# Kernel optimization log

Hardware: AMD Instinct MI355X
Metric: run time of the kernel (lower is better)

The kernel has to match this reference:

```python
import math
import jax, jax.numpy as jnp
import numpy as np

B, S, D, H = 4, 1024, 512, 8
DH = D // H  # 64
SQRT_DIM = math.sqrt(D)


def _relative_shift(pos_score):
    # pos_score: [B, H, S, S]
    b, h, s1, s2 = pos_score.shape
    zeros = jnp.zeros((b, h, s1, 1), dtype=pos_score.dtype)
    padded = jnp.concatenate([zeros, pos_score], axis=-1)      # [B,H,S,S+1]
    padded = padded.reshape(b, h, s2 + 1, s1)                  # [B,H,S+1,S]
    return padded[:, :, 1:].reshape(b, h, s1, s2)


def setup_inputs() -> dict:
    key = jax.random.key(0)
    ks = jax.random.split(key, 14)
    std = 0.02
    inp = {
        "query": jax.random.normal(ks[0], (B, S, D), jnp.float32),
        "key": jax.random.normal(ks[1], (B, S, D), jnp.float32),
        "value": jax.random.normal(ks[2], (B, S, D), jnp.float32),
        "pos_embedding": jax.random.normal(ks[3], (B, S, D), jnp.float32),
        # projection weights stored [in, out] so y = x @ W + b
        "Wq": jax.random.normal(ks[4], (D, D), jnp.float32) * std,
        "bq": jnp.zeros((D,), jnp.float32),
        "Wk": jax.random.normal(ks[5], (D, D), jnp.float32) * std,
        "bk": jnp.zeros((D,), jnp.float32),
        "Wv": jax.random.normal(ks[6], (D, D), jnp.float32) * std,
        "bv": jnp.zeros((D,), jnp.float32),
        "Wp": jax.random.normal(ks[7], (D, D), jnp.float32) * std,  # pos_proj, no bias
        "Wo": jax.random.normal(ks[8], (D, D), jnp.float32) * std,
        "bo": jnp.zeros((D,), jnp.float32),
        "u_bias": jax.random.normal(ks[9], (H, DH), jnp.float32) * std,
        "v_bias": jax.random.normal(ks[10], (H, DH), jnp.float32) * std,
    }
    return inp


def reference(query, key, value, pos_embedding, Wq, bq, Wk, bk, Wv, bv, Wp, Wo, bo, u_bias, v_bias):
    b = query.shape[0]
    q = (query @ Wq + bq).reshape(b, -1, H, DH)          # [B,S,H,DH]
    k = (key @ Wk + bk).reshape(b, -1, H, DH)            # [B,T,H,DH]
    v = (value @ Wv + bv).reshape(b, -1, H, DH)          # [B,T,H,DH]
    p = (pos_embedding @ Wp).reshape(b, -1, H, DH)       # [B,T,H,DH]

    # content score: (q + u) . k  -> [B,H,S,T]
    content_score = jnp.einsum('bshd,bthd->bhst', q + u_bias, k)
    # position score: (q + v) . pos -> [B,H,S,T], then relative shift
    pos_score = jnp.einsum('bshd,bthd->bhst', q + v_bias, p)
    pos_score = _relative_shift(pos_score)

    score = (content_score + pos_score) / SQRT_DIM
    attn = jax.nn.softmax(score, axis=-1)                # dropout p=0 (eval)

    context = jnp.einsum('bhst,bthd->bshd', attn, v).reshape(b, -1, D)
    out = context @ Wo + bo
    return (out, attn)
```

## Files before the change

kernel.cpp:

```cpp
#include <hip/hip_runtime.h>

#define B_  4
#define S_  1024
#define D_  512
#define H_  8
#define DH_ 64
#define SCALE 0.044194173824159216f

typedef short bf16x8 __attribute__((ext_vector_type(8)));
typedef float f32x4  __attribute__((ext_vector_type(4)));

__device__ __forceinline__ unsigned short f2bf(float x) {
    union { float f; unsigned int u; } v; v.f = x;
    unsigned int r = v.u + 0x7fffu + ((v.u >> 16) & 1u);
    return (unsigned short)(r >> 16);
}
__device__ __forceinline__ float bf2f(unsigned short h) {
    union { unsigned int u; float f; } v; v.u = ((unsigned int)h) << 16;
    return v.f;
}

__global__ __launch_bounds__(256) void convert_wt_k(
    const float* __restrict__ W0, const float* __restrict__ W1,
    const float* __restrict__ W2, const float* __restrict__ W3,
    const float* __restrict__ W4,
    unsigned short* __restrict__ T0, unsigned short* __restrict__ T1,
    unsigned short* __restrict__ T2, unsigned short* __restrict__ T3,
    unsigned short* __restrict__ T4)
{
    __shared__ float tile[64][65];
    const float* W;
    unsigned short* T;
    switch (blockIdx.z) {
        case 0: W = W0; T = T0; break;
        case 1: W = W1; T = T1; break;
        case 2: W = W2; T = T2; break;
        case 3: W = W3; T = T3; break;
        default: W = W4; T = T4; break;
    }
    const int r0 = blockIdx.y * 64, c0 = blockIdx.x * 64;
    const int tx = threadIdx.x & 63, ty = threadIdx.x >> 6;
#pragma unroll
    for (int it = 0; it < 16; ++it)
        tile[ty + 4 * it][tx] = W[(size_t)(r0 + ty + 4 * it) * 512 + c0 + tx];
    __syncthreads();
#pragma unroll
    for (int it = 0; it < 16; ++it)
        T[(size_t)(c0 + ty + 4 * it) * 512 + r0 + tx] = f2bf(tile[tx][ty + 4 * it]);
}

__global__ __launch_bounds__(256) void proj_all_k(
    const float* __restrict__ Aq_, const float* __restrict__ Ak_,
    const float* __restrict__ Ap_, const float* __restrict__ Av_,
    const unsigned short* __restrict__ WqT, const unsigned short* __restrict__ WkT,
    const unsigned short* __restrict__ WpT, const unsigned short* __restrict__ WvT,
    const float* __restrict__ bq, const float* __restrict__ bk,
    const float* __restrict__ bv,
    const float* __restrict__ ub, const float* __restrict__ vb,
    unsigned short* __restrict__ qu, unsigned short* __restrict__ qv,
    unsigned short* __restrict__ kbf, unsigned short* __restrict__ pbf,
    unsigned short* __restrict__ v2)
{
    __shared__ unsigned short Ab[64][72];
    __shared__ unsigned short Bb[64][72];
    const int mode = blockIdx.z;
    const float* A;
    const unsigned short* BT;
    switch (mode) {
        case 0: A = Aq_; BT = WqT; break;
        case 1: A = Ak_; BT = WkT; break;
        case 2: A = Ap_; BT = WpT; break;
        default: A = Av_; BT = WvT; break;
    }
    const int tid = threadIdx.x;
    const int i0 = blockIdx.x * 64, j0 = blockIdx.y * 64;
    const int w = tid >> 6, lane = tid & 63, l15 = lane & 15, lhi = lane >> 4;
    const int mr0 = (w >> 1) * 32, nc0 = (w & 1) * 32;
    f32x4 acc[2][2] = {};

    for (int k0 = 0; k0 < 512; k0 += 64) {
        __syncthreads();
#pragma unroll
        for (int it = 0; it < 4; ++it) {
            const int s = tid + it * 256;
            const int row = s >> 4, f4 = (s & 15) * 4;
            float4 va = *(const float4*)&A[(size_t)(i0 + row) * 512 + k0 + f4];
            ushort4 hh;
            hh.x = f2bf(va.x); hh.y = f2bf(va.y); hh.z = f2bf(va.z); hh.w = f2bf(va.w);
            *(ushort4*)&Ab[row][f4] = hh;
        }
#pragma unroll
        for (int it = 0; it < 2; ++it) {
            const int s = tid + it * 256;
            const int row = s >> 3, g = (s & 7) * 8;
            *(bf16x8*)&Bb[row][g] = *(const bf16x8*)&BT[(size_t)(j0 + row) * 512 + k0 + g];
        }
        __syncthreads();
#pragma unroll
        for (int kk = 0; kk < 2; ++kk) {
            bf16x8 a0 = *(const bf16x8*)&Ab[mr0 + l15][kk * 32 + lhi * 8];
            bf16x8 a1 = *(const bf16x8*)&Ab[mr0 + 16 + l15][kk * 32 + lhi * 8];
            bf16x8 b0 = *(const bf16x8*)&Bb[nc0 + l15][kk * 32 + lhi * 8];
            bf16x8 b1 = *(const bf16x8*)&Bb[nc0 + 16 + l15][kk * 32 + lhi * 8];
            acc[0][0] = __builtin_amdgcn_mfma_f32_16x16x32_bf16(a0, b0, acc[0][0], 0, 0, 0);
            acc[0][1] = __builtin_amdgcn_mfma_f32_16x16x32_bf16(a0, b1, acc[0][1], 0, 0, 0);
            acc[1][0] = __builtin_amdgcn_mfma_f32_16x16x32_bf16(a1, b0, acc[1][0], 0, 0, 0);
            acc[1][1] = __builtin_amdgcn_mfma_f32_16x16x32_bf16(a1, b1, acc[1][1], 0, 0, 0);
        }
    }

#pragma unroll
    for (int m = 0; m < 2; ++m)
#pragma unroll
        for (int n = 0; n < 2; ++n)
#pragma unroll
            for (int r = 0; r < 4; ++r) {
                const int grow = i0 + mr0 + 16 * m + 4 * lhi + r;
                const int gcol = j0 + nc0 + 16 * n + l15;
                const int b = grow >> 10, s = grow & 1023;
                const int h = gcol >> 6, d = gcol & 63;
                const float v = acc[m][n][r];
                if (mode == 3) {
                    const size_t idx = (((size_t)(b * H_ + h) * 32 + (s >> 5)) * 64 + d) * 32 + (s & 31);
                    v2[idx] = f2bf(v + bv[gcol]);
                } else {
                    const size_t idx = (((size_t)b * H_ + h) * S_ + s) * DH_ + d;
                    if (mode == 0) {
                        const float base = v + bq[gcol];
                        qu[idx] = f2bf(base + ub[gcol]);
                        qv[idx] = f2bf(base + vb[gcol]);
                    } else if (mode == 1) {
                        kbf[idx] = f2bf(v + bk[gcol]);
                    } else {
                        pbf[idx] = f2bf(v);
                    }
                }
            }
}

__global__ __launch_bounds__(256) void gemm_bf16_k(
    const unsigned short* __restrict__ A,
    const unsigned short* __restrict__ BT,
    const float* __restrict__ bias,
    float* __restrict__ C)
{
    __shared__ unsigned short Ab[64][72];
    __shared__ unsigned short Bb[64][72];
    const int tid = threadIdx.x;
    const int i0 = blockIdx.x * 64, j0 = blockIdx.y * 64;
    const int w = tid >> 6, lane = tid & 63, l15 = lane & 15, lhi = lane >> 4;
    const int mr0 = (w >> 1) * 32, nc0 = (w & 1) * 32;
    f32x4 acc[2][2] = {};

    for (int k0 = 0; k0 < 512; k0 += 64) {
        __syncthreads();
#pragma unroll
        for (int it = 0; it < 2; ++it) {
            const int s = tid + it * 256;
            const int row = s >> 3, g = (s & 7) * 8;
            *(bf16x8*)&Ab[row][g] = *(const bf16x8*)&A[(size_t)(i0 + row) * 512 + k0 + g];
            *(bf16x8*)&Bb[row][g] = *(const bf16x8*)&BT[(size_t)(j0 + row) * 512 + k0 + g];
        }
        __syncthreads();
#pragma unroll
        for (int kk = 0; kk < 2; ++kk) {
            bf16x8 a0 = *(const bf16x8*)&Ab[mr0 + l15][kk * 32 + lhi * 8];
            bf16x8 a1 = *(const bf16x8*)&Ab[mr0 + 16 + l15][kk * 32 + lhi * 8];
            bf16x8 b0 = *(const bf16x8*)&Bb[nc0 + l15][kk * 32 + lhi * 8];
            bf16x8 b1 = *(const bf16x8*)&Bb[nc0 + 16 + l15][kk * 32 + lhi * 8];
            acc[0][0] = __builtin_amdgcn_mfma_f32_16x16x32_bf16(a0, b0, acc[0][0], 0, 0, 0);
            acc[0][1] = __builtin_amdgcn_mfma_f32_16x16x32_bf16(a0, b1, acc[0][1], 0, 0, 0);
            acc[1][0] = __builtin_amdgcn_mfma_f32_16x16x32_bf16(a1, b0, acc[1][0], 0, 0, 0);
            acc[1][1] = __builtin_amdgcn_mfma_f32_16x16x32_bf16(a1, b1, acc[1][1], 0, 0, 0);
        }
    }

#pragma unroll
    for (int m = 0; m < 2; ++m)
#pragma unroll
        for (int n = 0; n < 2; ++n)
#pragma unroll
            for (int r = 0; r < 4; ++r) {
                const int grow = i0 + mr0 + 16 * m + 4 * lhi + r;
                const int gcol = j0 + nc0 + 16 * n + l15;
                C[(size_t)grow * 512 + gcol] = acc[m][n][r] + bias[gcol];
            }
}

#define RS 1032
#define QBLK 16

__global__ __launch_bounds__(512, 4) void score_fused_k(
    const unsigned short* __restrict__ qu_g,
    const unsigned short* __restrict__ qv_g,
    const unsigned short* __restrict__ kb_g,
    const unsigned short* __restrict__ pb_g,
    const unsigned short* __restrict__ v2_g,
    float* __restrict__ attn,
    unsigned short* __restrict__ ctx_g)
{
    __shared__ unsigned short Kb[128][72];
    __shared__ unsigned short Pb[128][72];
    __shared__ unsigned short Rsh[16 * RS];
    __shared__ float red[16][9];

    const int tid = threadIdx.x;
    const int i0 = blockIdx.x * QBLK;
    const int bh = blockIdx.y;
    const int w = tid >> 6, lane = tid & 63, l15 = lane & 15, lhi = lane >> 4;

    const unsigned short* qu_b = qu_g + (size_t)bh * S_ * DH_;
    const unsigned short* qv_b = qv_g + (size_t)bh * S_ * DH_;
    const unsigned short* kb_b = kb_g + (size_t)bh * S_ * DH_;
    const unsigned short* pb_b = pb_g + (size_t)bh * S_ * DH_;

    if (tid < 16) {
        const int j = i0 + tid + 1;
        if (j <= 1023) Rsh[tid * RS + j] = 0;
    }

    bf16x8 qf[2], aq0[2], aq1[2];
    {
        const int qrow  = i0 + l15;
        const int qrow1 = min(i0 + 16 + l15, S_ - 1);
#pragma unroll
        for (int kk = 0; kk < 2; ++kk) {
            const int off = kk * 32 + lhi * 8;
            qf[kk]  = *(const bf16x8*)&qu_b[(size_t)qrow  * DH_ + off];
            aq0[kk] = *(const bf16x8*)&qv_b[(size_t)qrow  * DH_ + off];
            aq1[kk] = *(const bf16x8*)&qv_b[(size_t)qrow1 * DH_ + off];
        }
    }

    bf16x8 kreg[2], preg[2];
#pragma unroll
    for (int it = 0; it < 2; ++it) {
        const int s = tid + it * 512;
        const int row = s >> 3, seg = (s & 7) * 8;
        kreg[it] = *(const bf16x8*)&kb_b[(size_t)row * DH_ + seg];
        preg[it] = *(const bf16x8*)&pb_b[(size_t)row * DH_ + seg];
    }

    f32x4 acc[8] = {};
    for (int jc = 0; jc < 8; ++jc) {
        __syncthreads();
#pragma unroll
        for (int it = 0; it < 2; ++it) {
            const int s = tid + it * 512;
            const int row = s >> 3, seg = (s & 7) * 8;
            *(bf16x8*)&Kb[row][seg] = kreg[it];
            *(bf16x8*)&Pb[row][seg] = preg[it];
        }
        if (jc < 7) {
#pragma unroll
            for (int it = 0; it < 2; ++it) {
                const int s = tid + it * 512;
                const int row = (jc + 1) * 128 + (s >> 3), seg = (s & 7) * 8;
                kreg[it] = *(const bf16x8*)&kb_b[(size_t)row * DH_ + seg];
                preg[it] = *(const bf16x8*)&pb_b[(size_t)row * DH_ + seg];
            }
        }
        __syncthreads();

        f32x4 racc0 = {}, racc1 = {};
#pragma unroll
        for (int kk = 0; kk < 2; ++kk) {
            bf16x8 pfr = *(const bf16x8*)&Pb[16 * w + l15][kk * 32 + lhi * 8];
            bf16x8 kfr = *(const bf16x8*)&Kb[16 * w + l15][kk * 32 + lhi * 8];
            racc0 = __builtin_amdgcn_mfma_f32_16x16x32_bf16(aq0[kk], pfr, racc0, 0, 0, 0);
            racc1 = __builtin_amdgcn_mfma_f32_16x16x32_bf16(aq1[kk], pfr, racc1, 0, 0, 0);
            acc[jc] = __builtin_amdgcn_mfma_f32_16x16x32_bf16(qf[kk], kfr, acc[jc], 0, 0, 0);
        }

        const int u = jc * 128 + 16 * w + l15;
#pragma unroll
        for (int r = 0; r < 4; ++r) {
            const int rl = 4 * lhi + r;
            const int gr = i0 + rl;
            const int jlo = u + gr - 1023;
            const unsigned short val = f2bf(racc0[r]);
            if (jlo >= 0)      Rsh[rl * RS + jlo] = val;
            else if (rl >= 1)  Rsh[(rl - 1) * RS + (u + gr + 1)] = val;
        }
        if (lhi == 0) {
            const int jhi = u + i0 + 17;
            if (jhi <= 1023) Rsh[15 * RS + jhi] = f2bf(racc1[0]);
        }
    }
    __syncthreads();

    const int il = 4 * lhi;
    float rmax[4], rsum[4];
#pragma unroll
    for (int r = 0; r < 4; ++r) rmax[r] = -3.0e38f;

#pragma unroll
    for (int jc = 0; jc < 8; ++jc)
#pragma unroll
        for (int r = 0; r < 4; ++r) {
            const int row = il + r;
            const int j = jc * 128 + 16 * w + l15;
            const float pos = bf2f(Rsh[row * RS + j]);
            const float s = (acc[jc][r] + pos) * SCALE;
            acc[jc][r] = s;
            rmax[r] = fmaxf(rmax[r], s);
        }

#pragma unroll
    for (int r = 0; r < 4; ++r)
#pragma unroll
        for (int off = 1; off < 16; off <<= 1)
            rmax[r] = fmaxf(rmax[r], __shfl_xor(rmax[r], off));
    if (l15 == 0)
#pragma unroll
        for (int r = 0; r < 4; ++r) red[il + r][w] = rmax[r];
    __syncthreads();
#pragma unroll
    for (int r = 0; r < 4; ++r) {
        float mx = red[il + r][0];
#pragma unroll
        for (int ww = 1; ww < 8; ++ww) mx = fmaxf(mx, red[il + r][ww]);
        rmax[r] = mx;
        rsum[r] = 0.f;
    }
    __syncthreads();

#pragma unroll
    for (int jc = 0; jc < 8; ++jc)
#pragma unroll
        for (int r = 0; r < 4; ++r) {
            const float e = __expf(acc[jc][r] - rmax[r]);
            acc[jc][r] = e;
            rsum[r] += e;
        }
#pragma unroll
    for (int r = 0; r < 4; ++r)
#pragma unroll
        for (int off = 1; off < 16; off <<= 1)
            rsum[r] += __shfl_xor(rsum[r], off);
    if (l15 == 0)
#pragma unroll
        for (int r = 0; r < 4; ++r) red[il + r][w] = rsum[r];
    __syncthreads();

    float* attn_b = attn + (size_t)bh * S_ * S_;
#pragma unroll
    for (int r = 0; r < 4; ++r) {
        float sum = red[il + r][0];
#pragma unroll
        for (int ww = 1; ww < 8; ++ww) sum += red[il + r][ww];
        const float inv = 1.f / sum;
#pragma unroll
        for (int jc = 0; jc < 8; ++jc) {
            const int j = jc * 128 + 16 * w + l15;
            const float pn = acc[jc][r] * inv;
            attn_b[(size_t)(i0 + il + r) * S_ + j] = pn;
            Rsh[(il + r) * RS + j] = f2bf(pn);
        }
    }
    __syncthreads();

    const int b4 = bh >> 3, h4 = bh & 7;
    const int nblk = w & 3;
    const int kh = w >> 2;
    const unsigned short* v2b = v2_g + (size_t)bh * 32 * 2048;
    const int dd = 16 * nblk + l15;
    f32x4 cacc = {};
#pragma unroll
    for (int half = 0; half < 2; ++half) {
        bf16x8 bbuf[8];
#pragma unroll
        for (int ki = 0; ki < 8; ++ki) {
            const int tb = kh * 16 + half * 8 + ki;
            bbuf[ki] = *(const bf16x8*)&v2b[(size_t)tb * 2048 + dd * 32 + lhi * 8];
        }
#pragma unroll
        for (int ki = 0; ki < 8; ++ki) {
            const int t0 = (kh * 16 + half * 8 + ki) * 32 + lhi * 8;
            bf16x8 a = *(const bf16x8*)&Rsh[l15 * RS + t0];
            cacc = __builtin_amdgcn_mfma_f32_16x16x32_bf16(a, bbuf[ki], cacc, 0, 0, 0);
        }
    }
    float* fred = (float*)&Kb[0][0];
    if (kh == 0) {
#pragma unroll
        for (int r = 0; r < 4; ++r)
            fred[(nblk * 16 + 4 * lhi + r) * 16 + l15] = cacc[r];
    }
    __syncthreads();
    if (kh == 1) {
#pragma unroll
        for (int r = 0; r < 4; ++r) {
            const float vs = cacc[r] + fred[(nblk * 16 + 4 * lhi + r) * 16 + l15];
            const int srow = i0 + 4 * lhi + r;
            ctx_g[((size_t)(b4 * S_ + srow)) * D_ + h4 * DH_ + 16 * nblk + l15] = f2bf(vs);
        }
    }
}

extern "C" void kernel_launch(void* const* d_in, const int* in_sizes, int n_in,
                              void* d_out, int out_size, void* d_ws, size_t ws_size,
                              hipStream_t stream)
{
    const float* query = (const float*)d_in[0];
    const float* key_  = (const float*)d_in[1];
    const float* value = (const float*)d_in[2];
    const float* pose  = (const float*)d_in[3];
    const float* Wq = (const float*)d_in[4];
    const float* bq = (const float*)d_in[5];
    const float* Wk = (const float*)d_in[6];
    const float* bk = (const float*)d_in[7];
    const float* Wv = (const float*)d_in[8];
    const float* bv = (const float*)d_in[9];
    const float* Wp = (const float*)d_in[10];
    const float* Wo = (const float*)d_in[11];
    const float* bo = (const float*)d_in[12];
    const float* u_bias = (const float*)d_in[13];
    const float* v_bias = (const float*)d_in[14];

    const size_t NTOK = (size_t)B_ * S_ * D_;
    float* out  = (float*)d_out;
    float* attn = (float*)d_out + NTOK;

    unsigned short* qu  = (unsigned short*)d_ws;
    unsigned short* qv  = qu + NTOK;
    unsigned short* kbf = qv + NTOK;
    unsigned short* pbf = kbf + NTOK;
    unsigned short* WqT = pbf + NTOK;
    unsigned short* WkT = WqT + 262144;
    unsigned short* WpT = WkT + 262144;
    unsigned short* WvT = WpT + 262144;
    unsigned short* WoT = WvT + 262144;
    unsigned short* v2  = WoT + 262144;
    unsigned short* ctx = v2 + NTOK;

    const dim3 blk256(256);
    const dim3 gproj(64, 8);

    convert_wt_k<<<dim3(8, 8, 5), blk256, 0, stream>>>(Wq, Wk, Wp, Wv, Wo,
                                                       WqT, WkT, WpT, WvT, WoT);

    proj_all_k<<<dim3(64, 8, 4), blk256, 0, stream>>>(
        query, key_, pose, value,
        WqT, WkT, WpT, WvT,
        bq, bk, bv, u_bias, v_bias,
        qu, qv, kbf, pbf, v2);

    score_fused_k<<<dim3(S_ / QBLK, B_ * H_), dim3(512), 0, stream>>>(
        qu, qv, kbf, pbf, v2, attn, ctx);

    gemm_bf16_k<<<gproj, blk256, 0, stream>>>(ctx, WoT, bo, out);
}
```

Measured before the change: 131.8 us.

## Enlarge projection tiles and load K/P fragments directly into registers

The projection GEMM now uses 128x128 tiles with 512 threads, each wave computing 2x4 MFMA tiles, so each loaded fragment is reused more often and fewer blocks are launched. The score kernel no longer stages K and P through shared memory with barriers per chunk. Each wave reads its own MFMA fragments from global memory straight into registers and prefetches the next chunk one step ahead. This cuts LDS traffic and barriers and shrinks shared memory, at the cost of less coalesced global reads and more registers.

```diff
diff --git a/kernel.cpp b/kernel.cpp
--- a/kernel.cpp
+++ b/kernel.cpp
@@ -49,7 +49,7 @@
         T[(size_t)(c0 + ty + 4 * it) * 512 + r0 + tx] = f2bf(tile[tx][ty + 4 * it]);
 }
 
-__global__ __launch_bounds__(256) void proj_all_k(
+__global__ __launch_bounds__(512) void proj_all_k(
     const float* __restrict__ Aq_, const float* __restrict__ Ak_,
     const float* __restrict__ Ap_, const float* __restrict__ Av_,
     const unsigned short* __restrict__ WqT, const unsigned short* __restrict__ WkT,
@@ -61,8 +61,8 @@
     unsigned short* __restrict__ kbf, unsigned short* __restrict__ pbf,
     unsigned short* __restrict__ v2)
 {
-    __shared__ unsigned short Ab[64][72];
-    __shared__ unsigned short Bb[64][72];
+    __shared__ unsigned short Ab[128][72];
+    __shared__ unsigned short Bb[128][72];
     const int mode = blockIdx.z;
     const float* A;
     const unsigned short* BT;
@@ -73,16 +73,16 @@
         default: A = Av_; BT = WvT; break;
     }
     const int tid = threadIdx.x;
-    const int i0 = blockIdx.x * 64, j0 = blockIdx.y * 64;
+    const int i0 = blockIdx.x * 128, j0 = blockIdx.y * 128;
     const int w = tid >> 6, lane = tid & 63, l15 = lane & 15, lhi = lane >> 4;
-    const int mr0 = (w >> 1) * 32, nc0 = (w & 1) * 32;
-    f32x4 acc[2][2] = {};
+    const int mr0 = (w >> 1) * 32, nc0 = (w & 1) * 64;
+    f32x4 acc[2][4] = {};
 
     for (int k0 = 0; k0 < 512; k0 += 64) {
         __syncthreads();
 #pragma unroll
         for (int it = 0; it < 4; ++it) {
-            const int s = tid + it * 256;
+            const int s = tid + it * 512;
             const int row = s >> 4, f4 = (s & 15) * 4;
             float4 va = *(const float4*)&A[(size_t)(i0 + row) * 512 + k0 + f4];
             ushort4 hh;
@@ -91,7 +91,7 @@
         }
 #pragma unroll
         for (int it = 0; it < 2; ++it) {
-            const int s = tid + it * 256;
+            const int s = tid + it * 512;
             const int row = s >> 3, g = (s & 7) * 8;
             *(bf16x8*)&Bb[row][g] = *(const bf16x8*)&BT[(size_t)(j0 + row) * 512 + k0 + g];
         }
@@ -100,19 +100,19 @@
         for (int kk = 0; kk < 2; ++kk) {
             bf16x8 a0 = *(const bf16x8*)&Ab[mr0 + l15][kk * 32 + lhi * 8];
             bf16x8 a1 = *(const bf16x8*)&Ab[mr0 + 16 + l15][kk * 32 + lhi * 8];
-            bf16x8 b0 = *(const bf16x8*)&Bb[nc0 + l15][kk * 32 + lhi * 8];
-            bf16x8 b1 = *(const bf16x8*)&Bb[nc0 + 16 + l15][kk * 32 + lhi * 8];
-            acc[0][0] = __builtin_amdgcn_mfma_f32_16x16x32_bf16(a0, b0, acc[0][0], 0, 0, 0);
-            acc[0][1] = __builtin_amdgcn_mfma_f32_16x16x32_bf16(a0, b1, acc[0][1], 0, 0, 0);
-            acc[1][0] = __builtin_amdgcn_mfma_f32_16x16x32_bf16(a1, b0, acc[1][0], 0, 0, 0);
-            acc[1][1] = __builtin_amdgcn_mfma_f32_16x16x32_bf16(a1, b1, acc[1][1], 0, 0, 0);
+#pragma unroll
+            for (int n = 0; n < 4; ++n) {
+                bf16x8 bn = *(const bf16x8*)&Bb[nc0 + 16 * n + l15][kk * 32 + lhi * 8];
+                acc[0][n] = __builtin_amdgcn_mfma_f32_16x16x32_bf16(a0, bn, acc[0][n], 0, 0, 0);
+                acc[1][n] = __builtin_amdgcn_mfma_f32_16x16x32_bf16(a1, bn, acc[1][n], 0, 0, 0);
+            }
         }
     }
 
 #pragma unroll
     for (int m = 0; m < 2; ++m)
 #pragma unroll
-        for (int n = 0; n < 2; ++n)
+        for (int n = 0; n < 4; ++n)
 #pragma unroll
             for (int r = 0; r < 4; ++r) {
                 const int grow = i0 + mr0 + 16 * m + 4 * lhi + r;
@@ -199,10 +199,9 @@
     float* __restrict__ attn,
     unsigned short* __restrict__ ctx_g)
 {
-    __shared__ unsigned short Kb[128][72];
-    __shared__ unsigned short Pb[128][72];
     __shared__ unsigned short Rsh[16 * RS];
     __shared__ float red[16][9];
+    __shared__ float fred[1024];
 
     const int tid = threadIdx.x;
     const int i0 = blockIdx.x * QBLK;
@@ -232,45 +231,34 @@
         }
     }
 
-    bf16x8 kreg[2], preg[2];
-#pragma unroll
-    for (int it = 0; it < 2; ++it) {
-        const int s = tid + it * 512;
-        const int row = s >> 3, seg = (s & 7) * 8;
-        kreg[it] = *(const bf16x8*)&kb_b[(size_t)row * DH_ + seg];
-        preg[it] = *(const bf16x8*)&pb_b[(size_t)row * DH_ + seg];
-    }
+    const unsigned short* kp = kb_b + (size_t)(16 * w + l15) * DH_ + lhi * 8;
+    const unsigned short* pp = pb_b + (size_t)(16 * w + l15) * DH_ + lhi * 8;
+
+    bf16x8 kc0 = *(const bf16x8*)kp;
+    bf16x8 kc1 = *(const bf16x8*)(kp + 32);
+    bf16x8 pc0 = *(const bf16x8*)pp;
+    bf16x8 pc1 = *(const bf16x8*)(pp + 32);
 
     f32x4 acc[8] = {};
+#pragma unroll
     for (int jc = 0; jc < 8; ++jc) {
-        __syncthreads();
-#pragma unroll
-        for (int it = 0; it < 2; ++it) {
-            const int s = tid + it * 512;
-            const int row = s >> 3, seg = (s & 7) * 8;
-            *(bf16x8*)&Kb[row][seg] = kreg[it];
-            *(bf16x8*)&Pb[row][seg] = preg[it];
-        }
+        bf16x8 kn0, kn1, pn0, pn1;
         if (jc < 7) {
-#pragma unroll
-            for (int it = 0; it < 2; ++it) {
-                const int s = tid + it * 512;
-                const int row = (jc + 1) * 128 + (s >> 3), seg = (s & 7) * 8;
-                kreg[it] = *(const bf16x8*)&kb_b[(size_t)row * DH_ + seg];
-                preg[it] = *(const bf16x8*)&pb_b[(size_t)row * DH_ + seg];
-            }
-        }
-        __syncthreads();
+            const unsigned short* kq = kp + (size_t)(jc + 1) * 128 * DH_;
+            const unsigned short* pq = pp + (size_t)(jc + 1) * 128 * DH_;
+            kn0 = *(const bf16x8*)kq;
+            kn1 = *(const bf16x8*)(kq + 32);
+            pn0 = *(const bf16x8*)pq;
+            pn1 = *(const bf16x8*)(pq + 32);
+        }
 
         f32x4 racc0 = {}, racc1 = {};
-#pragma unroll
-        for (int kk = 0; kk < 2; ++kk) {
-            bf16x8 pfr = *(const bf16x8*)&Pb[16 * w + l15][kk * 32 + lhi * 8];
-            bf16x8 kfr = *(const bf16x8*)&Kb[16 * w + l15][kk * 32 + lhi * 8];
-            racc0 = __builtin_amdgcn_mfma_f32_16x16x32_bf16(aq0[kk], pfr, racc0, 0, 0, 0);
-            racc1 = __builtin_amdgcn_mfma_f32_16x16x32_bf16(aq1[kk], pfr, racc1, 0, 0, 0);
-            acc[jc] = __builtin_amdgcn_mfma_f32_16x16x32_bf16(qf[kk], kfr, acc[jc], 0, 0, 0);
-        }
+        racc0 = __builtin_amdgcn_mfma_f32_16x16x32_bf16(aq0[0], pc0, racc0, 0, 0, 0);
+        racc0 = __builtin_amdgcn_mfma_f32_16x16x32_bf16(aq0[1], pc1, racc0, 0, 0, 0);
+        racc1 = __builtin_amdgcn_mfma_f32_16x16x32_bf16(aq1[0], pc0, racc1, 0, 0, 0);
+        racc1 = __builtin_amdgcn_mfma_f32_16x16x32_bf16(aq1[1], pc1, racc1, 0, 0, 0);
+        acc[jc] = __builtin_amdgcn_mfma_f32_16x16x32_bf16(qf[0], kc0, acc[jc], 0, 0, 0);
+        acc[jc] = __builtin_amdgcn_mfma_f32_16x16x32_bf16(qf[1], kc1, acc[jc], 0, 0, 0);
 
         const int u = jc * 128 + 16 * w + l15;
 #pragma unroll
@@ -286,6 +274,8 @@
             const int jhi = u + i0 + 17;
             if (jhi <= 1023) Rsh[15 * RS + jhi] = f2bf(racc1[0]);
         }
+
+        if (jc < 7) { kc0 = kn0; kc1 = kn1; pc0 = pn0; pc1 = pn1; }
     }
     __syncthreads();
 
@@ -381,7 +371,6 @@
             cacc = __builtin_amdgcn_mfma_f32_16x16x32_bf16(a, bbuf[ki], cacc, 0, 0, 0);
         }
     }
-    float* fred = (float*)&Kb[0][0];
     if (kh == 0) {
 #pragma unroll
         for (int r = 0; r < 4; ++r)
@@ -440,7 +429,7 @@
     convert_wt_k<<<dim3(8, 8, 5), blk256, 0, stream>>>(Wq, Wk, Wp, Wv, Wo,
                                                        WqT, WkT, WpT, WvT, WoT);
 
-    proj_all_k<<<dim3(64, 8, 4), blk256, 0, stream>>>(
+    proj_all_k<<<dim3(32, 4, 4), dim3(512), 0, stream>>>(
         query, key_, pose, value,
         WqT, WkT, WpT, WvT,
         bq, bk, bv, u_bias, v_bias,
```

Result: slower. 143.0 us (+8.5%).
